# Kernel optimization log

Hardware: AMD Instinct MI355X
Metric: run time of the kernel (lower is better)

## Reference

```python
import jax, jax.numpy as jnp
import numpy as np

BANDS = [[0,63],[48,111],[96,159],[144,207],[192,255],[240,303],[288,351],[336,399],[384,447],[432,495],[480,543],[528,591],[576,639],[624,687],[672,735],[720,783],[768,831],[816,879],[864,927],[912,975],[960,1023],[961,1024]]
N_FFT, WIN, HOP, FREQ = 2048, 2048, 512, 1025
B, T, D = 8, 2048, 128
NB = len(BANDS)
WIDTH = BANDS[0][1] - BANDS[0][0] + 1  # 64, all bands equal width
STARTS = np.array([s for s, _ in BANDS])
POS = STARTS[:, None] + np.arange(WIDTH)[None, :]  # (NB, WIDTH) freq-bin indices


def setup_inputs() -> dict:
    key = jax.random.key(0)
    k1, k2, k3 = jax.random.split(key, 3)
    z = jax.random.normal(k1, (B, T, NB, D), jnp.float32)
    mix_spec = jax.random.normal(k2, (B, 2, T, FREQ), jnp.float32)
    W = jax.random.normal(k3, (NB, D, WIDTH * 2), jnp.float32) * 1e-4  # init std=0.0001
    b = jnp.zeros((NB, WIDTH * 2), jnp.float32).at[:, 0::2].set(1.0)   # real part bias = 1
    return {"z": z, "mix_spec": mix_spec, "W": W, "b": b}


def _istft(spec_r, spec_i):
    # spec_r/spec_i: (B, T, F) -> waveform (B, HOP*(T-1)), center=True semantics
    comp = spec_r + 1j * spec_i
    frames = jnp.fft.irfft(comp, n=N_FFT, axis=-1)  # (B, T, n_fft)
    n = jnp.arange(WIN, dtype=frames.dtype)
    win = 0.5 * (1.0 - jnp.cos(2.0 * jnp.pi * n / WIN))  # periodic Hann
    frames = frames * win
    total = HOP * (T - 1) + N_FFT
    pos = HOP * jnp.arange(T)[:, None] + jnp.arange(N_FFT)[None, :]  # (T, n_fft)
    out = jnp.zeros((frames.shape[0], total), frames.dtype).at[:, pos].add(frames)
    env = jnp.zeros((total,), frames.dtype).at[pos].add(win * win)
    out = out / jnp.where(env > 1e-11, env, 1.0)
    start = N_FFT // 2
    return out[:, start:start + HOP * (T - 1)]


def reference(z, mix_spec, W, b):
    # per-band linear projections (all same width -> one batched einsum)
    band = jnp.einsum('btnd,ndo->btno', z, W) + b          # (B, T, NB, 2*WIDTH)
    band = band.reshape(B, T, NB, WIDTH, 2)
    # scatter-add into overlapping frequency ranges + overlap-count normalization
    mask = jnp.zeros((B, T, FREQ, 2), z.dtype).at[:, :, POS, :].add(band)
    wgt = jnp.zeros((FREQ,), z.dtype).at[POS].add(1.0)
    mask = mask / jnp.maximum(wgt, 1.0)[None, None, :, None]
    mask_r, mask_i = mask[..., 0], mask[..., 1]            # (B, T, F)
    mix_r, mix_i = mix_spec[:, 0], mix_spec[:, 1]          # (B, T, F)
    out_r = mask_r * mix_r - mask_i * mix_i
    out_i = mask_r * mix_i + mask_i * mix_r
    return _istft(out_r, out_i)
```

## Files before the change

kernel.cpp:

```cpp
#include <hip/hip_runtime.h>

typedef _Float16 f16x8 __attribute__((ext_vector_type(8)));
typedef _Float16 f16x2 __attribute__((ext_vector_type(2)));
typedef float f32x4 __attribute__((ext_vector_type(4)));

#define SLOT_DW 2048
#define WT_BYTE_OFF 134217728
#define PHYS(i) ((i) + ((i) >> 5))

__global__ __launch_bounds__(256) void k_init(const float* __restrict__ W,
                                              _Float16* __restrict__ Wt) {
  int n = blockIdx.x;
  int tid = threadIdx.x;
  __shared__ _Float16 L[128 * 130];
  const float* Wn = W + (size_t)n * 16384;
  for (int el = tid; el < 16384; el += 256) {
    int d = el >> 7, o = el & 127;
    L[d * 130 + o] = (_Float16)(Wn[el] * 4096.0f);
  }
  __syncthreads();
  _Float16* Wtn = Wt + (size_t)n * 16384;
  for (int el = tid; el < 16384; el += 256) {
    int o = el >> 7, d = el & 127;
    Wtn[el] = L[d * 130 + o];
  }
}

__global__ __launch_bounds__(256) void kA(const float* __restrict__ z,
                                          const _Float16* __restrict__ Wt,
                                          _Float16* __restrict__ band) {
  int mt = blockIdx.x;
  int n  = blockIdx.y;
  int r0 = mt * 64;
  __shared__ __align__(16) _Float16 Cs[64 * 136];
  int tid = threadIdx.x;
  int lane = tid & 63, wave = tid >> 6;
  int l16 = lane & 15, quad = lane >> 4;

  const _Float16* Wn = Wt + (size_t)n * 16384;
  f32x4 acc[2][4];
#pragma unroll
  for (int c = 0; c < 2; c++)
#pragma unroll
    for (int rt = 0; rt < 4; rt++) acc[c][rt] = (f32x4){0.f, 0.f, 0.f, 0.f};

#pragma unroll
  for (int kb = 0; kb < 4; kb++) {
    int ko = kb * 32 + quad * 8;
    f16x8 b0 = *(const f16x8*)(Wn + (wave * 32 + l16) * 128 + ko);
    f16x8 b1 = *(const f16x8*)(Wn + (wave * 32 + 16 + l16) * 128 + ko);
#pragma unroll
    for (int rt = 0; rt < 4; rt++) {
      const float* src = z + ((size_t)(r0 + rt * 16 + l16) * 22 + n) * 128 + ko;
      float4 v0 = *(const float4*)src;
      float4 v1 = *(const float4*)(src + 4);
      f16x8 a;
      a[0] = (_Float16)v0.x; a[1] = (_Float16)v0.y; a[2] = (_Float16)v0.z; a[3] = (_Float16)v0.w;
      a[4] = (_Float16)v1.x; a[5] = (_Float16)v1.y; a[6] = (_Float16)v1.z; a[7] = (_Float16)v1.w;
      acc[0][rt] = __builtin_amdgcn_mfma_f32_16x16x32_f16(a, b0, acc[0][rt], 0, 0, 0);
      acc[1][rt] = __builtin_amdgcn_mfma_f32_16x16x32_f16(a, b1, acc[1][rt], 0, 0, 0);
    }
  }
  const float inv_scale = 1.0f / 4096.0f;
#pragma unroll
  for (int c = 0; c < 2; c++) {
    int col = (wave * 2 + c) * 16 + l16;
#pragma unroll
    for (int rt = 0; rt < 4; rt++) {
#pragma unroll
      for (int reg = 0; reg < 4; reg++) {
        int row = rt * 16 + quad * 4 + reg;
        Cs[row * 136 + col] = (_Float16)(acc[c][rt][reg] * inv_scale);
      }
    }
  }
  __syncthreads();
  int row = tid >> 2;
  int c4 = (tid & 3) * 32;
  const _Float16* srcl = &Cs[row * 136 + c4];
  _Float16* dst = band + (size_t)(r0 + row) * (SLOT_DW * 2) + n * 128 + c4;
  f16x8 v0 = *(const f16x8*)(srcl);
  f16x8 v1 = *(const f16x8*)(srcl + 8);
  f16x8 v2 = *(const f16x8*)(srcl + 16);
  f16x8 v3 = *(const f16x8*)(srcl + 24);
  *(f16x8*)(dst)      = v0;
  *(f16x8*)(dst + 8)  = v1;
  *(f16x8*)(dst + 16) = v2;
  *(f16x8*)(dst + 24) = v3;
}

__global__ __launch_bounds__(256) void kB(const float* __restrict__ mix,
                                          const float* __restrict__ bias,
                                          float* __restrict__ ws) {
  int r = blockIdx.x;
  int b = r >> 11, t = r & 2047;
  __shared__ __align__(16) float2 bufA[1056];
  __shared__ __align__(16) float2 bufB[1056];
  int tid = threadIdx.x;

  const _Float16* bandg = (const _Float16*)(ws + (size_t)r * SLOT_DW);
  const float2* bias2 = (const float2*)bias;
  const float* mixr = mix + ((size_t)(b * 2) * 2048 + t) * 1025;
  const float* mixi = mix + ((size_t)(b * 2 + 1) * 2048 + t) * 1025;

  for (int k = tid; k <= 512; k += 256) {
    float2 X[2];
#pragma unroll
    for (int side = 0; side < 2; side++) {
      int f = side ? (1024 - k) : k;
      float mr = 0.f, mi = 0.f;
      int wgt = 0;
      int nhi = f / 48; if (nhi > 20) nhi = 20;
      int nlo = (f >= 16) ? (f - 16) / 48 : 0;
      for (int n = nlo; n <= nhi; n++) {
        int idx = n * 128 + 2 * (f - n * 48);
        f16x2 bv = *(const f16x2*)(bandg + idx);
        float2 bb = bias2[idx >> 1];
        mr += (float)bv[0] + bb.x;
        mi += (float)bv[1] + bb.y;
        wgt++;
      }
      if (f >= 961) {
        int idx = 21 * 128 + 2 * (f - 961);
        f16x2 bv = *(const f16x2*)(bandg + idx);
        float2 bb = bias2[idx >> 1];
        mr += (float)bv[0] + bb.x;
        mi += (float)bv[1] + bb.y;
        wgt++;
      }
      float inv = (wgt == 1) ? 1.0f : ((wgt == 2) ? 0.5f : (1.0f / 3.0f));
      mr *= inv; mi *= inv;
      float xr = mixr[f], xi = mixi[f];
      float outr = mr * xr - mi * xi;
      float outi = mr * xi + mi * xr;
      if (f == 0 || f == 1024) outi = 0.0f;
      X[side] = make_float2(outr, outi);
      if (k == 512) { X[1] = X[0]; break; }
    }
    float Ar = X[0].x + X[1].x, Ai = X[0].y - X[1].y;
    float Br = X[0].x - X[1].x, Bi = X[0].y + X[1].y;
    float sv, cv;
    __sincosf((float)k * 3.0679615757712823e-3f, &sv, &cv);
    float s1 = cv * Bi + sv * Br;
    float s2 = cv * Br - sv * Bi;
    bufA[PHYS(k & 1023)] = make_float2(Ar - s1, Ai + s2);
    if (k > 0 && k < 512) bufA[PHYS(1024 - k)] = make_float2(Ar + s1, -Ai + s2);
  }

  float2* src = bufA;
  float2* dst = bufB;
#pragma unroll
  for (int st = 0; st < 5; st++) {
    const int s = 2 * st;
    const int m = 1 << s;
    __syncthreads();
    int q = tid >> s, rr = tid & (m - 1);
    float2 x0 = src[PHYS(tid)];
    float2 x1 = src[PHYS(tid + 256)];
    float2 x2 = src[PHYS(tid + 512)];
    float2 x3 = src[PHYS(tid + 768)];
    float ang = (float)(q * m) * 6.135923151542565e-3f;
    float ws1, wc1;
    __sincosf(ang, &ws1, &wc1);
    float wc2 = wc1 * wc1 - ws1 * ws1, ws2 = 2.0f * wc1 * ws1;
    float wc3 = wc2 * wc1 - ws2 * ws1, ws3 = wc2 * ws1 + ws2 * wc1;
    float tAr = x0.x + x2.x, tAi = x0.y + x2.y;
    float tBr = x0.x - x2.x, tBi = x0.y - x2.y;
    float tCr = x1.x + x3.x, tCi = x1.y + x3.y;
    float tDr = x1.x - x3.x, tDi = x1.y - x3.y;
    int base = 4 * q * m + rr;
    dst[PHYS(base)] = make_float2(tAr + tCr, tAi + tCi);
    float pr = tBr - tDi, pi = tBi + tDr;
    dst[PHYS(base + m)] = make_float2(wc1 * pr - ws1 * pi, wc1 * pi + ws1 * pr);
    float qr = tAr - tCr, qi = tAi - tCi;
    dst[PHYS(base + 2 * m)] = make_float2(wc2 * qr - ws2 * qi, wc2 * qi + ws2 * qr);
    float rr2 = tBr + tDi, ri2 = tBi - tDr;
    dst[PHYS(base + 3 * m)] = make_float2(wc3 * rr2 - ws3 * ri2, wc3 * ri2 + ws3 * rr2);
    float2* tmp = src; src = dst; dst = tmp;
  }
  __syncthreads();

  float2* slot2 = (float2*)(ws + (size_t)r * SLOT_DW);
  const float inv_n = 1.0f / 2048.0f;
  for (int j = tid; j < 1024; j += 256) {
    float2 g = src[PHYS(j)];
    float c0 = __cosf((float)(2 * j) * 3.0679615757712823e-3f);
    float c1 = __cosf((float)(2 * j + 1) * 3.0679615757712823e-3f);
    float w0 = 0.5f * (1.0f - c0);
    float w1 = 0.5f * (1.0f - c1);
    slot2[j] = make_float2(g.x * inv_n * w0, g.y * inv_n * w1);
  }
}

__global__ __launch_bounds__(256) void kC(const float* __restrict__ ws,
                                          float* __restrict__ out) {
  int b = blockIdx.y;
  int p = blockIdx.x * 256 + threadIdx.x;
  int q = p + 1024;
  int t0 = (q - 1536) >> 9; if (t0 < 0) t0 = 0;
  int t1 = q >> 9;          if (t1 > 2047) t1 = 2047;
  float sum = 0.f;
  for (int t = t0; t <= t1; t++) {
    int i = q - (t << 9);
    sum += ws[(size_t)(b * 2048 + t) * SLOT_DW + i];
  }
  float env;
  if (t1 - t0 == 3) {
    env = 1.5f;
  } else {
    env = 0.f;
    for (int t = t0; t <= t1; t++) {
      int i = q - (t << 9);
      float c = __cosf((float)i * 3.0679615757712823e-3f);
      float win = 0.5f * (1.0f - c);
      env += win * win;
    }
  }
  out[(size_t)b * 1048064 + p] = sum / (env > 1e-11f ? env : 1.0f);
}

extern "C" void kernel_launch(void* const* d_in, const int* in_sizes, int n_in,
                              void* d_out, int out_size, void* d_ws, size_t ws_size,
                              hipStream_t stream) {
  const float* z    = (const float*)d_in[0];
  const float* mix  = (const float*)d_in[1];
  const float* W    = (const float*)d_in[2];
  const float* bias = (const float*)d_in[3];
  float* out = (float*)d_out;
  _Float16* Wt = (_Float16*)((char*)d_ws + WT_BYTE_OFF);

  k_init<<<22, 256, 0, stream>>>(W, Wt);
  kA<<<dim3(256, 22), 256, 0, stream>>>(z, Wt, (_Float16*)d_ws);
  kB<<<16384, 256, 0, stream>>>(mix, bias, (float*)d_ws);
  kC<<<dim3(4094, 8), 256, 0, stream>>>((const float*)d_ws, out);
}
```

Before: 532.4 us.

## Stage z tile in LDS via async global_load_lds and split weight transpose

The GEMM kernel now copies each 64x128 fp32 z tile into shared memory with direct global-to-LDS async loads, using padded row pairs. Previously every wave re-read the same z rows from global memory. Weight fragments are preloaded into registers, and the weight transpose kernel is split across four blocks per band so it runs on more CUs. The trade-off is extra LDS use (about 33KB), which can lower occupancy, plus an added barrier.

Measured after the change: 487.7 us. -8.4%, faster.

```diff
diff --git a/kernel.cpp b/kernel.cpp
--- a/kernel.cpp
+++ b/kernel.cpp
@@ -8,21 +8,26 @@
 #define WT_BYTE_OFF 134217728
 #define PHYS(i) ((i) + ((i) >> 5))
 
+__device__ __forceinline__ void async_copy16(const void* g, void* l) {
+  __builtin_amdgcn_global_load_lds((const __attribute__((address_space(1))) void*)g,
+                                   (__attribute__((address_space(3))) void*)l, 16, 0, 0);
+}
+
 __global__ __launch_bounds__(256) void k_init(const float* __restrict__ W,
                                               _Float16* __restrict__ Wt) {
-  int n = blockIdx.x;
+  int n = blockIdx.x >> 2, dq = blockIdx.x & 3;
   int tid = threadIdx.x;
-  __shared__ _Float16 L[128 * 130];
-  const float* Wn = W + (size_t)n * 16384;
-  for (int el = tid; el < 16384; el += 256) {
-    int d = el >> 7, o = el & 127;
-    L[d * 130 + o] = (_Float16)(Wn[el] * 4096.0f);
-  }
-  __syncthreads();
-  _Float16* Wtn = Wt + (size_t)n * 16384;
-  for (int el = tid; el < 16384; el += 256) {
-    int o = el >> 7, d = el & 127;
-    Wtn[el] = L[d * 130 + o];
+  __shared__ _Float16 L[32 * 130];
+  const float* Wn = W + (size_t)n * 16384 + dq * 32 * 128;
+  for (int el = tid; el < 4096; el += 256) {
+    int dl = el >> 7, o = el & 127;
+    L[dl * 130 + o] = (_Float16)(Wn[el] * 4096.0f);
+  }
+  __syncthreads();
+  _Float16* Wtn = Wt + (size_t)n * 16384 + dq * 32;
+  for (int el = tid; el < 4096; el += 256) {
+    int o = el >> 5, dl = el & 31;
+    Wtn[o * 128 + dl] = L[dl * 130 + o];
   }
 }
 
@@ -32,35 +37,56 @@
   int mt = blockIdx.x;
   int n  = blockIdx.y;
   int r0 = mt * 64;
-  __shared__ __align__(16) _Float16 Cs[64 * 136];
+  __shared__ __align__(16) char smem[33280];
   int tid = threadIdx.x;
   int lane = tid & 63, wave = tid >> 6;
   int l16 = lane & 15, quad = lane >> 4;
 
   const _Float16* Wn = Wt + (size_t)n * 16384;
-  f32x4 acc[2][4];
-#pragma unroll
-  for (int c = 0; c < 2; c++)
-#pragma unroll
-    for (int rt = 0; rt < 4; rt++) acc[c][rt] = (f32x4){0.f, 0.f, 0.f, 0.f};
-
+  f16x8 bfrag[8];
 #pragma unroll
   for (int kb = 0; kb < 4; kb++) {
     int ko = kb * 32 + quad * 8;
-    f16x8 b0 = *(const f16x8*)(Wn + (wave * 32 + l16) * 128 + ko);
-    f16x8 b1 = *(const f16x8*)(Wn + (wave * 32 + 16 + l16) * 128 + ko);
+    bfrag[2 * kb]     = *(const f16x8*)(Wn + (wave * 32 + l16) * 128 + ko);
+    bfrag[2 * kb + 1] = *(const f16x8*)(Wn + (wave * 32 + 16 + l16) * 128 + ko);
+  }
+
+  {
+    int col16 = lane & 31;
+    int rowh  = lane >> 5;
+#pragma unroll
+    for (int it = 0; it < 8; it++) {
+      int pr = wave * 8 + it;
+      const float* g = z + ((size_t)(r0 + 2 * pr + rowh) * 22 + n) * 128 + col16 * 4;
+      async_copy16(g, smem + pr * 1040);
+    }
+  }
+  __syncthreads();
+
+  f32x4 acc[2][4];
+#pragma unroll
+  for (int c = 0; c < 2; c++)
+#pragma unroll
+    for (int rt = 0; rt < 4; rt++) acc[c][rt] = (f32x4){0.f, 0.f, 0.f, 0.f};
+
+#pragma unroll
+  for (int kb = 0; kb < 4; kb++) {
 #pragma unroll
     for (int rt = 0; rt < 4; rt++) {
-      const float* src = z + ((size_t)(r0 + rt * 16 + l16) * 22 + n) * 128 + ko;
-      float4 v0 = *(const float4*)src;
-      float4 v1 = *(const float4*)(src + 4);
+      int row = rt * 16 + l16;
+      const float* ap = (const float*)(smem + (row >> 1) * 1040 + (row & 1) * 512) + kb * 32 + quad * 8;
+      float4 v0 = *(const float4*)ap;
+      float4 v1 = *(const float4*)(ap + 4);
       f16x8 a;
       a[0] = (_Float16)v0.x; a[1] = (_Float16)v0.y; a[2] = (_Float16)v0.z; a[3] = (_Float16)v0.w;
       a[4] = (_Float16)v1.x; a[5] = (_Float16)v1.y; a[6] = (_Float16)v1.z; a[7] = (_Float16)v1.w;
-      acc[0][rt] = __builtin_amdgcn_mfma_f32_16x16x32_f16(a, b0, acc[0][rt], 0, 0, 0);
-      acc[1][rt] = __builtin_amdgcn_mfma_f32_16x16x32_f16(a, b1, acc[1][rt], 0, 0, 0);
-    }
-  }
+      acc[0][rt] = __builtin_amdgcn_mfma_f32_16x16x32_f16(a, bfrag[2 * kb],     acc[0][rt], 0, 0, 0);
+      acc[1][rt] = __builtin_amdgcn_mfma_f32_16x16x32_f16(a, bfrag[2 * kb + 1], acc[1][rt], 0, 0, 0);
+    }
+  }
+  __syncthreads();
+
+  _Float16* Cs = (_Float16*)smem;
   const float inv_scale = 1.0f / 4096.0f;
 #pragma unroll
   for (int c = 0; c < 2; c++) {
@@ -229,7 +255,7 @@
   float* out = (float*)d_out;
   _Float16* Wt = (_Float16*)((char*)d_ws + WT_BYTE_OFF);
 
-  k_init<<<22, 256, 0, stream>>>(W, Wt);
+  k_init<<<88, 256, 0, stream>>>(W, Wt);
   kA<<<dim3(256, 22), 256, 0, stream>>>(z, Wt, (_Float16*)d_ws);
   kB<<<16384, 256, 0, stream>>>(mix, bias, (float*)d_ws);
   kC<<<dim3(4094, 8), 256, 0, stream>>>((const float*)d_ws, out);
```
